# Optimization experiments

Measured on AMD Instinct MI355X. Metric: run time of the kernel, lower is better.

## Reference

```python
import jax, jax.numpy as jnp
import numpy as np

N_VOX = 500000
P, S, K = 2048, 64, 8          # pixels(rays), samples per ray, voxel neighbors per sample
F_M, F_H = 64, 128             # voxel feature dim, mlp hidden dim
FREQ_PE = 4
DEPTH_MIN, DEPTH_MAX = 1.0, 80.0
RAY_SAMPLE_STEPS = 64.0
EPS = 1e-10
IN_FEAT = F_M + 3 * FREQ_PE * 2  # 88


def lrelu(x):
    return jnp.where(x >= 0, x, 0.1 * x)  # LeakyReLU(0.1)


def posenc(x, L=FREQ_PE):
    # NeRF positional encoding: sin/cos(2^i * x), i in [0, L)
    freqs = 2.0 ** jnp.arange(L, dtype=x.dtype)          # [L]
    ang = x[..., None] * freqs                            # [..., 3, L]
    enc = jnp.concatenate([jnp.sin(ang), jnp.cos(ang)], axis=-1)  # [..., 3, 2L]
    return enc.reshape(x.shape[:-1] + (x.shape[-1] * 2 * L,))


def setup_inputs() -> dict:
    key = jax.random.key(0)
    ks = jax.random.split(key, 16)

    def xavier(k, fan_in, fan_out):
        return jax.random.normal(k, (fan_in, fan_out), jnp.float32) / np.sqrt(fan_in)

    inp = {
        'map_xyz': jax.random.normal(ks[0], (N_VOX, 3), jnp.float32),
        'map_feat': jax.random.normal(ks[1], (N_VOX, F_M), jnp.float32) * 0.05,
        'ind_voxel': jax.random.randint(ks[2], (P, S, K), 0, N_VOX),
        'sample_xyz': jax.random.normal(ks[3], (P, S, 3), jnp.float32),
        'dist_to_cam': jax.random.uniform(ks[4], (P, S), jnp.float32) * RAY_SAMPLE_STEPS,
        'W0': xavier(ks[5], IN_FEAT, F_H), 'b0': jnp.full((F_H,), 0.01, jnp.float32),
        'W1': xavier(ks[6], F_H, F_H),     'b1': jnp.full((F_H,), 0.01, jnp.float32),
        'W2': xavier(ks[7], F_H, F_H),     'b2': jnp.full((F_H,), 0.01, jnp.float32),
        'Wa0': xavier(ks[8], F_H, F_H // 2), 'ba0': jnp.full((F_H // 2,), 0.01, jnp.float32),
        'Wa1': xavier(ks[9], F_H // 2, 1),   'ba1': jnp.full((1,), 0.01, jnp.float32),
        'Wr0': xavier(ks[10], F_H, F_H // 2), 'br0': jnp.full((F_H // 2,), 0.01, jnp.float32),
        'Wr1': xavier(ks[11], F_H // 2, 3),   'br1': jnp.full((3,), 0.01, jnp.float32),
    }
    return inp


def reference(map_xyz, map_feat, ind_voxel, sample_xyz, dist_to_cam,
              W0, b0, W1, b1, W2, b2, Wa0, ba0, Wa1, ba1, Wr0, br0, Wr1, br1):
    # ---- voxel -> sample messages (func_msg_voxel_to_sample) ----
    voxel_xyz = map_xyz[ind_voxel]                       # [P,S,K,3] gather
    feat = map_feat[ind_voxel]                           # [P,S,K,F_M] gather
    offset = sample_xyz[:, :, None, :] - voxel_xyz       # [P,S,K,3]
    h = jnp.concatenate([feat, posenc(offset)], axis=-1) # [P,S,K,88]
    h = lrelu(h @ W0 + b0)
    h = lrelu(h @ W1 + b1)
    h = lrelu(h @ W2 + b2)                               # [P,S,K,F_H]
    w = jnp.exp(-10.0 * jnp.linalg.norm(offset, axis=-1))  # [P,S,K]
    w = w / jnp.sum(w, axis=-1, keepdims=True)
    # ---- reduce over K neighbors (func_reduce_voxel_to_sample) ----
    feat_s = jnp.sum(h * w[..., None], axis=2)           # [P,S,F_H]
    a = lrelu(feat_s @ Wa0 + ba0)
    alpha = jax.nn.sigmoid(a @ Wa1 + ba1)                # [P,S,1]
    r = lrelu(feat_s @ Wr0 + br0)
    rgb = jax.nn.sigmoid(r @ Wr1 + br1)                  # [P,S,3]
    # ---- sample -> pixel volume rendering (func_reduce_sample_to_pixel) ----
    dist = DEPTH_MIN + DEPTH_MAX * dist_to_cam / RAY_SAMPLE_STEPS  # [P,S]
    ones = jnp.ones((P, 1, 1), alpha.dtype)
    trans = jnp.cumprod(jnp.concatenate([ones, 1.0 - alpha + EPS], axis=1), axis=1)[:, :-1, :]
    blend = alpha * trans                                # [P,S,1]
    pixel_rgb = jnp.sum(rgb * blend, axis=1)             # [P,3]
    pixel_d = jnp.sum(dist[..., None] * blend, axis=1)   # [P,1]
    acc = jnp.sum(blend, axis=1)                         # [P,1]
    return jnp.concatenate([pixel_rgb, pixel_d, acc], axis=-1)  # [P,5]
```

## Files before the change

kernel.cpp:

```cpp
#include <hip/hip_runtime.h>

typedef __bf16 bf16_t;
typedef __bf16 bf16x4 __attribute__((ext_vector_type(4)));
typedef __bf16 bf16x8 __attribute__((ext_vector_type(8)));
typedef float  f32x4  __attribute__((ext_vector_type(4)));

#define NPIX 2048
#define NS   64
#define NK   8
#define NSAMP (NPIX*NS)
#define NROWS (NSAMP*NK)
#define TROWS 64
#define NTILES (NROWS/TROWS)
#define XSTR 104
#define HSTR 136

#define PK_W0 0
#define PK_W1 1536
#define PK_W2 3584
#define PK_WA 5632
#define PK_WR 6656
#define PK_TOT 7680

#define WS_AR_BYTES 122880

__global__ void pack_weights(const float* __restrict__ W0, const float* __restrict__ W1,
                             const float* __restrict__ W2, const float* __restrict__ Wa0,
                             const float* __restrict__ Wr0, bf16_t* __restrict__ dst0) {
  int tid = blockIdx.x * blockDim.x + threadIdx.x;
  if (tid >= PK_TOT * 8) return;
  const float* src; bf16_t* dst; int e, KD, ND, KS;
  if (tid < 12288)      { src = W0;  dst = dst0;         e = tid;         KD = 88;  ND = 128; KS = 3; }
  else if (tid < 28672) { src = W1;  dst = dst0 + 12288; e = tid - 12288; KD = 128; ND = 128; KS = 4; }
  else if (tid < 45056) { src = W2;  dst = dst0 + 28672; e = tid - 28672; KD = 128; ND = 128; KS = 4; }
  else if (tid < 53248) { src = Wa0; dst = dst0 + 45056; e = tid - 45056; KD = 128; ND = 64;  KS = 4; }
  else                  { src = Wr0; dst = dst0 + 53248; e = tid - 53248; KD = 128; ND = 64;  KS = 4; }
  int j = e & 7, l = (e >> 3) & 63, f = e >> 9;
  int s = f % KS, t = f / KS;
  int row = s * 32 + (l >> 4) * 8 + j;
  int col = t * 16 + (l & 15);
  float v = (row < KD) ? src[row * ND + col] : 0.f;
  dst[e] = (bf16_t)v;
}

__device__ __forceinline__ float lrelu(float v) { return fmaxf(v, 0.1f * v); }
__device__ __forceinline__ float sigmoidf(float x) { return 1.f / (1.f + __expf(-x)); }

__global__ __launch_bounds__(512, 4)
void nerf_main(const float* __restrict__ map_xyz, const float* __restrict__ map_feat,
               const int* __restrict__ ind, const float* __restrict__ sample_xyz,
               const float* __restrict__ b0g, const float* __restrict__ b1g,
               const float* __restrict__ b2g, const float* __restrict__ ba0g,
               const float* __restrict__ wa1g, const float* __restrict__ ba1g,
               const float* __restrict__ br0g, const float* __restrict__ wr1g,
               const float* __restrict__ br1g, const bf16_t* __restrict__ wpack,
               float* __restrict__ ar_out)
{
  __shared__ __align__(16) bf16_t sBuf[TROWS * HSTR];
  __shared__ __align__(16) bf16_t sHa[TROWS * HSTR];
  __shared__ __align__(16) bf16_t sFS[16 * HSTR];
  __shared__ __align__(16) bf16_t sAR[16 * HSTR];
  __shared__ __align__(16) bf16_t sFB[2048];
  __shared__ __align__(16) float sWt[TROWS];
  __shared__ float sWs[8];

  const int tid = threadIdx.x;
  const int wid = tid >> 6, l = tid & 63;
  const int q = l >> 4, n = l & 15;

  const bf16x8* pk = (const bf16x8*)wpack;
  bf16x8 w0f[3], w1f[4], w2f[4], hdf[4];
#pragma unroll
  for (int s = 0; s < 3; s++) w0f[s] = pk[PK_W0 + (wid * 3 + s) * 64 + l];
#pragma unroll
  for (int s = 0; s < 4; s++) w1f[s] = pk[PK_W1 + (wid * 4 + s) * 64 + l];
#pragma unroll
  for (int s = 0; s < 4; s++) w2f[s] = pk[PK_W2 + (wid * 4 + s) * 64 + l];
#pragma unroll
  for (int s = 0; s < 4; s++)
    hdf[s] = pk[(wid < 4 ? PK_WA : PK_WR) + ((wid & 3) * 4 + s) * 64 + l];

  const float4 b0v = *(const float4*)(b0g + wid * 16 + q * 4);
  const float4 b1v = *(const float4*)(b1g + wid * 16 + q * 4);
  const float4 b2v = *(const float4*)(b2g + wid * 16 + q * 4);
  const float4 bHv = *(const float4*)((wid < 4 ? ba0g : br0g) + (wid & 3) * 16 + q * 4);
  float4 fbv; fbv.x = br1g[0]; fbv.y = br1g[1]; fbv.z = br1g[2]; fbv.w = ba1g[0];

  for (int i = tid; i < 8 * HSTR; i += 512) {
    sFS[8 * HSTR + i] = (bf16_t)0.f;
    sAR[8 * HSTR + i] = (bf16_t)0.f;
  }
  {
    int e0 = tid * 4;
    int jb = e0 & 7, ll = (e0 >> 3) & 63, s = e0 >> 9;
    int m = ll & 15;
#pragma unroll
    for (int ii = 0; ii < 4; ii++) {
      int k = s * 32 + (ll >> 4) * 8 + jb + ii;
      float v = 0.f;
      if (k < 64)  { if (m < 3) v = wr1g[k * 3 + m]; }
      else         { if (m == 3) v = wa1g[k - 64]; }
      sFB[e0 + ii] = (bf16_t)v;
    }
  }
  __syncthreads();

  for (int tile = blockIdx.x; tile < NTILES; tile += gridDim.x) {
    const int m0 = tile * TROWS;

    {
      const int r = tid >> 3, p = tid & 7;
      const int m = m0 + r;
      const int idx = ind[m];
      const float4* fp = (const float4*)(map_feat + (size_t)idx * 64 + p * 8);
      float4 f0 = fp[0], f1 = fp[1];
      bf16x8 v;
      v[0] = (bf16_t)f0.x; v[1] = (bf16_t)f0.y; v[2] = (bf16_t)f0.z; v[3] = (bf16_t)f0.w;
      v[4] = (bf16_t)f1.x; v[5] = (bf16_t)f1.y; v[6] = (bf16_t)f1.z; v[7] = (bf16_t)f1.w;
      *(bf16x8*)(sBuf + r * XSTR + p * 8) = v;
      const int g = m >> 3;
      if (p < 6) {
        const int d = p >> 1;
        float o = sample_xyz[g * 3 + d] - map_xyz[idx * 3 + d];
        float s1 = __sinf(o), c1 = __cosf(o);
        float s2 = 2.f * s1 * c1, c2 = 1.f - 2.f * s1 * s1;
        float s4 = 2.f * s2 * c2, c4 = 1.f - 2.f * s2 * s2;
        float s8 = 2.f * s4 * c4, c8 = 1.f - 2.f * s4 * s4;
        bf16x4 e;
        if (p & 1) { e[0] = (bf16_t)c1; e[1] = (bf16_t)c2; e[2] = (bf16_t)c4; e[3] = (bf16_t)c8; }
        else       { e[0] = (bf16_t)s1; e[1] = (bf16_t)s2; e[2] = (bf16_t)s4; e[3] = (bf16_t)s8; }
        *(bf16x4*)(sBuf + r * XSTR + 64 + d * 8 + (p & 1) * 4) = e;
      } else if (p == 6) {
        bf16x8 z = {};
        *(bf16x8*)(sBuf + r * XSTR + 88) = z;
      } else {
        float ox = sample_xyz[g * 3 + 0] - map_xyz[idx * 3 + 0];
        float oy = sample_xyz[g * 3 + 1] - map_xyz[idx * 3 + 1];
        float oz = sample_xyz[g * 3 + 2] - map_xyz[idx * 3 + 2];
        sWt[r] = __expf(-10.f * sqrtf(ox * ox + oy * oy + oz * oz));
      }
    }
    __syncthreads();

    if (tid < 8) {
      float ss = 0.f;
#pragma unroll
      for (int k = 0; k < 8; k++) ss += sWt[tid * 8 + k];
      sWs[tid] = ss;
    }

    {
      f32x4 acc[4] = {};
#pragma unroll
      for (int st = 0; st < 4; st++)
#pragma unroll
        for (int s = 0; s < 3; s++) {
          bf16x8 b = *(const bf16x8*)(sBuf + (st * 16 + n) * XSTR + s * 32 + q * 8);
          acc[st] = __builtin_amdgcn_mfma_f32_16x16x32_bf16(w0f[s], b, acc[st], 0, 0, 0);
        }
#pragma unroll
      for (int st = 0; st < 4; st++) {
        bf16x4 o;
        o[0] = (bf16_t)lrelu(acc[st][0] + b0v.x);
        o[1] = (bf16_t)lrelu(acc[st][1] + b0v.y);
        o[2] = (bf16_t)lrelu(acc[st][2] + b0v.z);
        o[3] = (bf16_t)lrelu(acc[st][3] + b0v.w);
        *(bf16x4*)(sHa + (st * 16 + n) * HSTR + wid * 16 + q * 4) = o;
      }
    }
    __syncthreads();

    {
      f32x4 acc[4] = {};
#pragma unroll
      for (int st = 0; st < 4; st++)
#pragma unroll
        for (int s = 0; s < 4; s++) {
          bf16x8 b = *(const bf16x8*)(sHa + (st * 16 + n) * HSTR + s * 32 + q * 8);
          acc[st] = __builtin_amdgcn_mfma_f32_16x16x32_bf16(w1f[s], b, acc[st], 0, 0, 0);
        }
#pragma unroll
      for (int st = 0; st < 4; st++) {
        bf16x4 o;
        o[0] = (bf16_t)lrelu(acc[st][0] + b1v.x);
        o[1] = (bf16_t)lrelu(acc[st][1] + b1v.y);
        o[2] = (bf16_t)lrelu(acc[st][2] + b1v.z);
        o[3] = (bf16_t)lrelu(acc[st][3] + b1v.w);
        *(bf16x4*)(sBuf + (st * 16 + n) * HSTR + wid * 16 + q * 4) = o;
      }
    }
    __syncthreads();

    {
      f32x4 acc[4] = {};
#pragma unroll
      for (int st = 0; st < 4; st++)
#pragma unroll
        for (int s = 0; s < 4; s++) {
          bf16x8 b = *(const bf16x8*)(sBuf + (st * 16 + n) * HSTR + s * 32 + q * 8);
          acc[st] = __builtin_amdgcn_mfma_f32_16x16x32_bf16(w2f[s], b, acc[st], 0, 0, 0);
        }
#pragma unroll
      for (int st = 0; st < 4; st++) {
        bf16x4 o;
        o[0] = (bf16_t)lrelu(acc[st][0] + b2v.x);
        o[1] = (bf16_t)lrelu(acc[st][1] + b2v.y);
        o[2] = (bf16_t)lrelu(acc[st][2] + b2v.z);
        o[3] = (bf16_t)lrelu(acc[st][3] + b2v.w);
        *(bf16x4*)(sHa + (st * 16 + n) * HSTR + wid * 16 + q * 4) = o;
      }
    }
    __syncthreads();

    {
      int g = tid >> 6;
      int c = (tid & 63) * 2;
      float a0 = 0.f, a1 = 0.f;
#pragma unroll
      for (int k = 0; k < 8; k++) {
        float wk = sWt[g * 8 + k];
        unsigned u = *(const unsigned*)(sHa + (g * 8 + k) * HSTR + c);
        a0 += wk * __uint_as_float(u << 16);
        a1 += wk * __uint_as_float(u & 0xffff0000u);
      }
      float inv = 1.f / sWs[g];
      sFS[g * HSTR + c]     = (bf16_t)(a0 * inv);
      sFS[g * HSTR + c + 1] = (bf16_t)(a1 * inv);
    }
    __syncthreads();

    {
      f32x4 ha = {};
#pragma unroll
      for (int s = 0; s < 4; s++) {
        bf16x8 b = *(const bf16x8*)(sFS + n * HSTR + s * 32 + q * 8);
        ha = __builtin_amdgcn_mfma_f32_16x16x32_bf16(hdf[s], b, ha, 0, 0, 0);
      }
      if (n < 8) {
        const int base = (wid < 4) ? 64 : 0;
        bf16x4 o;
        o[0] = (bf16_t)lrelu(ha[0] + bHv.x);
        o[1] = (bf16_t)lrelu(ha[1] + bHv.y);
        o[2] = (bf16_t)lrelu(ha[2] + bHv.z);
        o[3] = (bf16_t)lrelu(ha[3] + bHv.w);
        *(bf16x4*)(sAR + n * HSTR + base + (wid & 3) * 16 + q * 4) = o;
      }
    }
    __syncthreads();

    if (wid == 0) {
      f32x4 c = {};
#pragma unroll
      for (int s = 0; s < 4; s++) {
        bf16x8 a = *(const bf16x8*)(sFB + (s * 64 + l) * 8);
        bf16x8 b = *(const bf16x8*)(sAR + n * HSTR + s * 32 + q * 8);
        c = __builtin_amdgcn_mfma_f32_16x16x32_bf16(a, b, c, 0, 0, 0);
      }
      if (q == 0 && n < 8) {
        float4 o;
        o.x = sigmoidf(c[0] + fbv.x);
        o.y = sigmoidf(c[1] + fbv.y);
        o.z = sigmoidf(c[2] + fbv.z);
        o.w = sigmoidf(c[3] + fbv.w);
        ((float4*)ar_out)[m0 / 8 + n] = o;
      }
    }
  }
}

__global__ __launch_bounds__(512)
void render_kernel(const float* __restrict__ ar, const float* __restrict__ dcam,
                   float* __restrict__ out) {
  int ray = blockIdx.x * 8 + (threadIdx.x >> 6);
  int s = threadIdx.x & 63;
  float4 v = ((const float4*)ar)[ray * 64 + s];
  float alpha = v.w;
  float t = 1.f - alpha + 1e-10f;
  float p = t;
#pragma unroll
  for (int d = 1; d < 64; d <<= 1) {
    float o = __shfl_up(p, d);
    if (s >= d) p *= o;
  }
  float pm1 = __shfl_up(p, 1);
  float T = (s == 0) ? 1.f : pm1;
  float bl = alpha * T;
  float dist = 1.f + 1.25f * dcam[ray * 64 + s];
  float cr = v.x * bl, cg = v.y * bl, cb = v.z * bl, cd = dist * bl, ca = bl;
#pragma unroll
  for (int d = 32; d > 0; d >>= 1) {
    cr += __shfl_xor(cr, d);
    cg += __shfl_xor(cg, d);
    cb += __shfl_xor(cb, d);
    cd += __shfl_xor(cd, d);
    ca += __shfl_xor(ca, d);
  }
  if (s == 0) {
    out[ray * 5 + 0] = cr; out[ray * 5 + 1] = cg; out[ray * 5 + 2] = cb;
    out[ray * 5 + 3] = cd; out[ray * 5 + 4] = ca;
  }
}

extern "C" void kernel_launch(void* const* d_in, const int* in_sizes, int n_in,
                              void* d_out, int out_size, void* d_ws, size_t ws_size,
                              hipStream_t stream) {
  const float* map_xyz    = (const float*)d_in[0];
  const float* map_feat   = (const float*)d_in[1];
  const int*   ind        = (const int*)d_in[2];
  const float* sample_xyz = (const float*)d_in[3];
  const float* dist_cam   = (const float*)d_in[4];
  const float* W0  = (const float*)d_in[5];
  const float* b0  = (const float*)d_in[6];
  const float* W1  = (const float*)d_in[7];
  const float* b1  = (const float*)d_in[8];
  const float* W2  = (const float*)d_in[9];
  const float* b2  = (const float*)d_in[10];
  const float* Wa0 = (const float*)d_in[11];
  const float* ba0 = (const float*)d_in[12];
  const float* Wa1 = (const float*)d_in[13];
  const float* ba1 = (const float*)d_in[14];
  const float* Wr0 = (const float*)d_in[15];
  const float* br0 = (const float*)d_in[16];
  const float* Wr1 = (const float*)d_in[17];
  const float* br1 = (const float*)d_in[18];

  bf16_t* wpack = (bf16_t*)d_ws;
  float*  ar    = (float*)((char*)d_ws + WS_AR_BYTES);

  pack_weights<<<240, 256, 0, stream>>>(W0, W1, W2, Wa0, Wr0, wpack);
  nerf_main<<<512, 512, 0, stream>>>(map_xyz, map_feat, ind, sample_xyz,
                                     b0, b1, b2, ba0, Wa1, ba1, br0, Wr1, br1,
                                     wpack, ar);
  render_kernel<<<256, 512, 0, stream>>>(ar, dist_cam, (float*)d_out);
}
```

Before: 401.8 us.

## Prefetch next tile's voxel gathers into registers and fold biases into MFMA accumulators

Gathers for the next tile (indices, map features, xyz) are issued into registers right after the input-staging barrier, so their latency overlaps the MLP MFMA chain of the current tile. Biases move into shared memory and are used to initialise the MFMA accumulators, which removes the separate bias adds and frees persistent registers. s_setprio brackets are added around the MFMA loops. The prefetch adds live registers under a 4-wave occupancy bound, which risks spills or lower occupancy.

New measurement: 409.9 us. 2.0% more time.

```diff
diff --git a/kernel.cpp b/kernel.cpp
--- a/kernel.cpp
+++ b/kernel.cpp
@@ -1,6 +1,7 @@
 #include <hip/hip_runtime.h>
 
 typedef __bf16 bf16_t;
+typedef __bf16 bf16x2 __attribute__((ext_vector_type(2)));
 typedef __bf16 bf16x4 __attribute__((ext_vector_type(4)));
 typedef __bf16 bf16x8 __attribute__((ext_vector_type(8)));
 typedef float  f32x4  __attribute__((ext_vector_type(4)));
@@ -63,10 +64,12 @@
   __shared__ __align__(16) bf16_t sFB[2048];
   __shared__ __align__(16) float sWt[TROWS];
   __shared__ float sWs[8];
+  __shared__ __align__(16) float sB0[128], sB1[128], sB2[128], sBH[128], sFBv[4];
 
   const int tid = threadIdx.x;
   const int wid = tid >> 6, l = tid & 63;
   const int q = l >> 4, n = l & 15;
+  const int sr = tid >> 3, sp = tid & 7;
 
   const bf16x8* pk = (const bf16x8*)wpack;
   bf16x8 w0f[3], w1f[4], w2f[4], hdf[4];
@@ -79,12 +82,6 @@
 #pragma unroll
   for (int s = 0; s < 4; s++)
     hdf[s] = pk[(wid < 4 ? PK_WA : PK_WR) + ((wid & 3) * 4 + s) * 64 + l];
-
-  const float4 b0v = *(const float4*)(b0g + wid * 16 + q * 4);
-  const float4 b1v = *(const float4*)(b1g + wid * 16 + q * 4);
-  const float4 b2v = *(const float4*)(b2g + wid * 16 + q * 4);
-  const float4 bHv = *(const float4*)((wid < 4 ? ba0g : br0g) + (wid & 3) * 16 + q * 4);
-  float4 fbv; fbv.x = br1g[0]; fbv.y = br1g[1]; fbv.z = br1g[2]; fbv.w = ba1g[0];
 
   for (int i = tid; i < 8 * HSTR; i += 512) {
     sFS[8 * HSTR + i] = (bf16_t)0.f;
@@ -103,44 +100,69 @@
       sFB[e0 + ii] = (bf16_t)v;
     }
   }
+  if (tid < 128)      sB0[tid] = b0g[tid];
+  else if (tid < 256) sB1[tid - 128] = b1g[tid - 128];
+  else if (tid < 384) sB2[tid - 256] = b2g[tid - 256];
+  else { int t = tid - 384; sBH[t] = (t < 64) ? ba0g[t] : br0g[t - 64]; }
+  if (tid < 4) sFBv[tid] = (tid < 3) ? br1g[tid] : ba1g[0];
   __syncthreads();
+
+  int   pidx = 0;
+  float4 pf0 = {}, pf1 = {};
+  float ps0 = 0.f, ps1 = 0.f, ps2 = 0.f, pm0 = 0.f, pm1 = 0.f, pm2 = 0.f;
+
+  auto prefetch = [&](int t) {
+    const int m = t * TROWS + sr;
+    pidx = ind[m];
+    const float4* fp = (const float4*)(map_feat + (size_t)pidx * 64 + sp * 8);
+    pf0 = fp[0]; pf1 = fp[1];
+    const int g = m >> 3;
+    if (sp < 6) {
+      const int d = sp >> 1;
+      ps0 = sample_xyz[g * 3 + d];
+      pm0 = map_xyz[pidx * 3 + d];
+    } else if (sp == 7) {
+      ps0 = sample_xyz[g * 3 + 0]; pm0 = map_xyz[pidx * 3 + 0];
+      ps1 = sample_xyz[g * 3 + 1]; pm1 = map_xyz[pidx * 3 + 1];
+      ps2 = sample_xyz[g * 3 + 2]; pm2 = map_xyz[pidx * 3 + 2];
+    }
+  };
+
+  prefetch(blockIdx.x);
 
   for (int tile = blockIdx.x; tile < NTILES; tile += gridDim.x) {
     const int m0 = tile * TROWS;
 
     {
-      const int r = tid >> 3, p = tid & 7;
-      const int m = m0 + r;
-      const int idx = ind[m];
-      const float4* fp = (const float4*)(map_feat + (size_t)idx * 64 + p * 8);
-      float4 f0 = fp[0], f1 = fp[1];
       bf16x8 v;
-      v[0] = (bf16_t)f0.x; v[1] = (bf16_t)f0.y; v[2] = (bf16_t)f0.z; v[3] = (bf16_t)f0.w;
-      v[4] = (bf16_t)f1.x; v[5] = (bf16_t)f1.y; v[6] = (bf16_t)f1.z; v[7] = (bf16_t)f1.w;
-      *(bf16x8*)(sBuf + r * XSTR + p * 8) = v;
-      const int g = m >> 3;
-      if (p < 6) {
-        const int d = p >> 1;
-        float o = sample_xyz[g * 3 + d] - map_xyz[idx * 3 + d];
+      v[0] = (bf16_t)pf0.x; v[1] = (bf16_t)pf0.y; v[2] = (bf16_t)pf0.z; v[3] = (bf16_t)pf0.w;
+      v[4] = (bf16_t)pf1.x; v[5] = (bf16_t)pf1.y; v[6] = (bf16_t)pf1.z; v[7] = (bf16_t)pf1.w;
+      *(bf16x8*)(sBuf + sr * XSTR + sp * 8) = v;
+      if (sp < 6) {
+        const int d = sp >> 1;
+        float o = ps0 - pm0;
         float s1 = __sinf(o), c1 = __cosf(o);
         float s2 = 2.f * s1 * c1, c2 = 1.f - 2.f * s1 * s1;
         float s4 = 2.f * s2 * c2, c4 = 1.f - 2.f * s2 * s2;
         float s8 = 2.f * s4 * c4, c8 = 1.f - 2.f * s4 * s4;
         bf16x4 e;
-        if (p & 1) { e[0] = (bf16_t)c1; e[1] = (bf16_t)c2; e[2] = (bf16_t)c4; e[3] = (bf16_t)c8; }
-        else       { e[0] = (bf16_t)s1; e[1] = (bf16_t)s2; e[2] = (bf16_t)s4; e[3] = (bf16_t)s8; }
-        *(bf16x4*)(sBuf + r * XSTR + 64 + d * 8 + (p & 1) * 4) = e;
-      } else if (p == 6) {
+        if (sp & 1) { e[0] = (bf16_t)c1; e[1] = (bf16_t)c2; e[2] = (bf16_t)c4; e[3] = (bf16_t)c8; }
+        else        { e[0] = (bf16_t)s1; e[1] = (bf16_t)s2; e[2] = (bf16_t)s4; e[3] = (bf16_t)s8; }
+        *(bf16x4*)(sBuf + sr * XSTR + 64 + d * 8 + (sp & 1) * 4) = e;
+      } else if (sp == 6) {
         bf16x8 z = {};
-        *(bf16x8*)(sBuf + r * XSTR + 88) = z;
+        *(bf16x8*)(sBuf + sr * XSTR + 88) = z;
       } else {
-        float ox = sample_xyz[g * 3 + 0] - map_xyz[idx * 3 + 0];
-        float oy = sample_xyz[g * 3 + 1] - map_xyz[idx * 3 + 1];
-        float oz = sample_xyz[g * 3 + 2] - map_xyz[idx * 3 + 2];
-        sWt[r] = __expf(-10.f * sqrtf(ox * ox + oy * oy + oz * oz));
-      }
-    }
-    __syncthreads();
+        float ox = ps0 - pm0, oy = ps1 - pm1, oz = ps2 - pm2;
+        sWt[sr] = __expf(-10.f * sqrtf(ox * ox + oy * oy + oz * oz));
+      }
+    }
+    __syncthreads();
+
+    {
+      int nt = tile + (int)gridDim.x;
+      if (nt < NTILES) prefetch(nt);
+    }
 
     if (tid < 8) {
       float ss = 0.f;
@@ -150,7 +172,9 @@
     }
 
     {
-      f32x4 acc[4] = {};
+      f32x4 b0i = *(const f32x4*)(sB0 + wid * 16 + q * 4);
+      f32x4 acc[4] = {b0i, b0i, b0i, b0i};
+      __builtin_amdgcn_s_setprio(1);
 #pragma unroll
       for (int st = 0; st < 4; st++)
 #pragma unroll
@@ -158,20 +182,23 @@
           bf16x8 b = *(const bf16x8*)(sBuf + (st * 16 + n) * XSTR + s * 32 + q * 8);
           acc[st] = __builtin_amdgcn_mfma_f32_16x16x32_bf16(w0f[s], b, acc[st], 0, 0, 0);
         }
+      __builtin_amdgcn_s_setprio(0);
 #pragma unroll
       for (int st = 0; st < 4; st++) {
         bf16x4 o;
-        o[0] = (bf16_t)lrelu(acc[st][0] + b0v.x);
-        o[1] = (bf16_t)lrelu(acc[st][1] + b0v.y);
-        o[2] = (bf16_t)lrelu(acc[st][2] + b0v.z);
-        o[3] = (bf16_t)lrelu(acc[st][3] + b0v.w);
+        o[0] = (bf16_t)lrelu(acc[st][0]);
+        o[1] = (bf16_t)lrelu(acc[st][1]);
+        o[2] = (bf16_t)lrelu(acc[st][2]);
+        o[3] = (bf16_t)lrelu(acc[st][3]);
         *(bf16x4*)(sHa + (st * 16 + n) * HSTR + wid * 16 + q * 4) = o;
       }
     }
     __syncthreads();
 
     {
-      f32x4 acc[4] = {};
+      f32x4 b1i = *(const f32x4*)(sB1 + wid * 16 + q * 4);
+      f32x4 acc[4] = {b1i, b1i, b1i, b1i};
+      __builtin_amdgcn_s_setprio(1);
 #pragma unroll
       for (int st = 0; st < 4; st++)
 #pragma unroll
@@ -179,20 +206,23 @@
           bf16x8 b = *(const bf16x8*)(sHa + (st * 16 + n) * HSTR + s * 32 + q * 8);
           acc[st] = __builtin_amdgcn_mfma_f32_16x16x32_bf16(w1f[s], b, acc[st], 0, 0, 0);
         }
+      __builtin_amdgcn_s_setprio(0);
 #pragma unroll
       for (int st = 0; st < 4; st++) {
         bf16x4 o;
-        o[0] = (bf16_t)lrelu(acc[st][0] + b1v.x);
-        o[1] = (bf16_t)lrelu(acc[st][1] + b1v.y);
-        o[2] = (bf16_t)lrelu(acc[st][2] + b1v.z);
-        o[3] = (bf16_t)lrelu(acc[st][3] + b1v.w);
+        o[0] = (bf16_t)lrelu(acc[st][0]);
+        o[1] = (bf16_t)lrelu(acc[st][1]);
+        o[2] = (bf16_t)lrelu(acc[st][2]);
+        o[3] = (bf16_t)lrelu(acc[st][3]);
         *(bf16x4*)(sBuf + (st * 16 + n) * HSTR + wid * 16 + q * 4) = o;
       }
     }
     __syncthreads();
 
     {
-      f32x4 acc[4] = {};
+      f32x4 b2i = *(const f32x4*)(sB2 + wid * 16 + q * 4);
+      f32x4 acc[4] = {b2i, b2i, b2i, b2i};
+      __builtin_amdgcn_s_setprio(1);
 #pragma unroll
       for (int st = 0; st < 4; st++)
 #pragma unroll
@@ -200,13 +230,14 @@
           bf16x8 b = *(const bf16x8*)(sBuf + (st * 16 + n) * HSTR + s * 32 + q * 8);
           acc[st] = __builtin_amdgcn_mfma_f32_16x16x32_bf16(w2f[s], b, acc[st], 0, 0, 0);
         }
+      __builtin_amdgcn_s_setprio(0);
 #pragma unroll
       for (int st = 0; st < 4; st++) {
         bf16x4 o;
-        o[0] = (bf16_t)lrelu(acc[st][0] + b2v.x);
-        o[1] = (bf16_t)lrelu(acc[st][1] + b2v.y);
-        o[2] = (bf16_t)lrelu(acc[st][2] + b2v.z);
-        o[3] = (bf16_t)lrelu(acc[st][3] + b2v.w);
+        o[0] = (bf16_t)lrelu(acc[st][0]);
+        o[1] = (bf16_t)lrelu(acc[st][1]);
+        o[2] = (bf16_t)lrelu(acc[st][2]);
+        o[3] = (bf16_t)lrelu(acc[st][3]);
         *(bf16x4*)(sHa + (st * 16 + n) * HSTR + wid * 16 + q * 4) = o;
       }
     }
@@ -224,32 +255,36 @@
         a1 += wk * __uint_as_float(u & 0xffff0000u);
       }
       float inv = 1.f / sWs[g];
-      sFS[g * HSTR + c]     = (bf16_t)(a0 * inv);
-      sFS[g * HSTR + c + 1] = (bf16_t)(a1 * inv);
-    }
-    __syncthreads();
-
-    {
-      f32x4 ha = {};
+      bf16x2 fo;
+      fo[0] = (bf16_t)(a0 * inv);
+      fo[1] = (bf16_t)(a1 * inv);
+      *(bf16x2*)(sFS + g * HSTR + c) = fo;
+    }
+    __syncthreads();
+
+    {
+      f32x4 ha = *(const f32x4*)(sBH + wid * 16 + q * 4);
+      __builtin_amdgcn_s_setprio(1);
 #pragma unroll
       for (int s = 0; s < 4; s++) {
         bf16x8 b = *(const bf16x8*)(sFS + n * HSTR + s * 32 + q * 8);
         ha = __builtin_amdgcn_mfma_f32_16x16x32_bf16(hdf[s], b, ha, 0, 0, 0);
       }
+      __builtin_amdgcn_s_setprio(0);
       if (n < 8) {
         const int base = (wid < 4) ? 64 : 0;
         bf16x4 o;
-        o[0] = (bf16_t)lrelu(ha[0] + bHv.x);
-        o[1] = (bf16_t)lrelu(ha[1] + bHv.y);
-        o[2] = (bf16_t)lrelu(ha[2] + bHv.z);
-        o[3] = (bf16_t)lrelu(ha[3] + bHv.w);
+        o[0] = (bf16_t)lrelu(ha[0]);
+        o[1] = (bf16_t)lrelu(ha[1]);
+        o[2] = (bf16_t)lrelu(ha[2]);
+        o[3] = (bf16_t)lrelu(ha[3]);
         *(bf16x4*)(sAR + n * HSTR + base + (wid & 3) * 16 + q * 4) = o;
       }
     }
     __syncthreads();
 
     if (wid == 0) {
-      f32x4 c = {};
+      f32x4 c = *(const f32x4*)sFBv;
 #pragma unroll
       for (int s = 0; s < 4; s++) {
         bf16x8 a = *(const bf16x8*)(sFB + (s * 64 + l) * 8);
@@ -258,10 +293,10 @@
       }
       if (q == 0 && n < 8) {
         float4 o;
-        o.x = sigmoidf(c[0] + fbv.x);
-        o.y = sigmoidf(c[1] + fbv.y);
-        o.z = sigmoidf(c[2] + fbv.z);
-        o.w = sigmoidf(c[3] + fbv.w);
+        o.x = sigmoidf(c[0]);
+        o.y = sigmoidf(c[1]);
+        o.z = sigmoidf(c[2]);
+        o.w = sigmoidf(c[3]);
         ((float4*)ar_out)[m0 / 8 + n] = o;
       }
     }
```
